# Optimization experiments

Hardware: AMD Instinct MI355X
Metric: run time of the kernel (lower is better)

## Reference

```python
import jax, jax.numpy as jnp
import numpy as np

LN_EPS = 1e-12

def setup_inputs() -> dict:
    key = jax.random.key(0)
    k1, k2 = jax.random.split(key)
    batch, seq_len, hidden, conv_size = 32, 2048, 512, 64
    input_tensor = jax.random.normal(k1, (batch, seq_len, hidden), dtype=jnp.float32)
    conv_weight = jax.random.normal(k2, (1, conv_size, hidden), dtype=jnp.float32) * 0.02
    gamma = jnp.ones((hidden,), dtype=jnp.float32)
    beta = jnp.zeros((hidden,), dtype=jnp.float32)
    return {"input_tensor": input_tensor, "conv_weight": conv_weight, "gamma": gamma, "beta": beta}

def reference(input_tensor, conv_weight, gamma, beta):
    # input_tensor: [B, S, H]; conv_weight: [1, K, H] (K << S)
    seq_len = input_tensor.shape[1]
    conv_size = conv_weight.shape[1]
    # FFT-based circular depthwise convolution along the sequence axis
    x_f = jnp.fft.rfft(input_tensor, axis=1, norm='ortho')            # [B, S//2+1, H] complex
    w_pad = jnp.pad(conv_weight, ((0, 0), (0, seq_len - conv_size), (0, 0)))  # zero-pad filter to S
    w_f = jnp.fft.rfft(w_pad, axis=1, norm='ortho')                   # [1, S//2+1, H]
    y = jnp.fft.irfft(x_f * w_f, n=seq_len, axis=1, norm='ortho')     # [B, S, H]
    # dropout is identity at inference; residual + LayerNorm(eps=1e-12)
    h = y + input_tensor
    mean = jnp.mean(h, axis=-1, keepdims=True)
    var = jnp.mean(jnp.square(h - mean), axis=-1, keepdims=True)
    return gamma * (h - mean) * jax.lax.rsqrt(var + LN_EPS) + beta
```

## Files before the change

kernel.cpp:

```cpp
#include <hip/hip_runtime.h>

#define S_LEN 2048
#define HDIM  512
#define KSZ   64
#define S_T   128
#define PH    16
#define INV_SQRT_S 0.02209708691207961f

struct Smem {
    float lh[2][PH][HDIM];
};

__device__ __forceinline__ void lds_barrier() {
    asm volatile("s_waitcnt lgkmcnt(0)\n\ts_barrier" ::: "memory");
}

template <int OFF, int BUF>
__device__ __forceinline__ void conv_phase(const float* __restrict__ xb, int sbase, int h,
                                           const float (&wr)[KSZ], float (&xw)[KSZ],
                                           float (&xp)[8], Smem* sm)
{
#pragma unroll
    for (int j = 0; j < PH; ++j) {
        const float xcur = xp[j & 7];
        xp[j & 7] = xb[((sbase + j + 8) & (S_LEN - 1)) * HDIM + h];

        float y0 = 0.f, y1 = 0.f, y2 = 0.f, y3 = 0.f;
#pragma unroll
        for (int k = 1; k <= KSZ - 7; k += 4) {
            y0 = fmaf(wr[k],     xw[(OFF + j - k)     & 63], y0);
            y1 = fmaf(wr[k + 1], xw[(OFF + j - k - 1) & 63], y1);
            y2 = fmaf(wr[k + 2], xw[(OFF + j - k - 2) & 63], y2);
            y3 = fmaf(wr[k + 3], xw[(OFF + j - k - 3) & 63], y3);
        }
        y0 = fmaf(wr[61], xw[(OFF + j - 61) & 63], y0);
        y1 = fmaf(wr[62], xw[(OFF + j - 62) & 63], y1);
        y2 = fmaf(wr[63], xw[(OFF + j - 63) & 63], y2);

        const float hval = fmaf(INV_SQRT_S, fmaf(wr[0], xcur, (y0 + y1) + (y2 + y3)), xcur);
        xw[(OFF + j) & 63] = xcur;
        sm->lh[BUF][j][h] = hval;
    }
}

template <int BUF>
__device__ __forceinline__ void ln_phase(int sbase, int lane, int wv,
                                         const float* __restrict__ gamma,
                                         const float* __restrict__ beta,
                                         float* __restrict__ ob, Smem* sm)
{
    lds_barrier();

    float gm[8], bt[8];
#pragma unroll
    for (int m = 0; m < 8; ++m) {
        gm[m] = gamma[lane + 64 * m];
        bt[m] = beta [lane + 64 * m];
    }

#pragma unroll
    for (int rr = 0; rr < 2; ++rr) {
        const int row = wv * 2 + rr;
        float v[8];
        float s = 0.f, q = 0.f;
#pragma unroll
        for (int m = 0; m < 8; ++m) {
            v[m] = sm->lh[BUF][row][lane + 64 * m];
            s += v[m];
            q = fmaf(v[m], v[m], q);
        }
#pragma unroll
        for (int d = 1; d < 64; d <<= 1) {
            s += __shfl_xor(s, d, 64);
            q += __shfl_xor(q, d, 64);
        }
        const float mean = s * (1.0f / 512.0f);
        const float rstd = rsqrtf(fmaf(q, 1.0f / 512.0f, -mean * mean) + 1e-12f);

        float* op = ob + (size_t)(sbase + row) * HDIM + lane;
#pragma unroll
        for (int m = 0; m < 8; ++m)
            op[64 * m] = fmaf(v[m] - mean, rstd * gm[m], bt[m]);
    }
}

__global__ __launch_bounds__(512, 2)
void fconv_ln(const float* __restrict__ x, const float* __restrict__ w,
              const float* __restrict__ gamma, const float* __restrict__ beta,
              float* __restrict__ out)
{
    __shared__ Smem sm;
    const int h    = threadIdx.x;
    const int lane = h & 63;
    const int wv   = h >> 6;
    const int b  = blockIdx.x >> 4;
    const int s0 = (blockIdx.x & 15) * S_T;

    const float* xb = x   + (size_t)b * S_LEN * HDIM;
    float*       ob = out + (size_t)b * S_LEN * HDIM;

    float wr[KSZ];
#pragma unroll
    for (int k = 0; k < KSZ; ++k) wr[k] = w[k * HDIM + h];

    float xw[KSZ];
#pragma unroll
    for (int d = 1; d < KSZ; ++d)
        xw[KSZ - d] = xb[((s0 - d) & (S_LEN - 1)) * HDIM + h];
    xw[0] = 0.f;

    float xp[8];
#pragma unroll
    for (int j = 0; j < 8; ++j) xp[j] = xb[(s0 + j) * HDIM + h];

    for (int grp = 0; grp < S_T / 64; ++grp) {
        const int base = s0 + grp * 64;
        conv_phase< 0, 0>(xb, base +  0, h, wr, xw, xp, &sm); ln_phase<0>(base +  0, lane, wv, gamma, beta, ob, &sm);
        conv_phase<16, 1>(xb, base + 16, h, wr, xw, xp, &sm); ln_phase<1>(base + 16, lane, wv, gamma, beta, ob, &sm);
        conv_phase<32, 0>(xb, base + 32, h, wr, xw, xp, &sm); ln_phase<0>(base + 32, lane, wv, gamma, beta, ob, &sm);
        conv_phase<48, 1>(xb, base + 48, h, wr, xw, xp, &sm); ln_phase<1>(base + 48, lane, wv, gamma, beta, ob, &sm);
    }
}

extern "C" void kernel_launch(void* const* d_in, const int* in_sizes, int n_in,
                              void* d_out, int out_size, void* d_ws, size_t ws_size,
                              hipStream_t stream) {
    const float* x  = (const float*)d_in[0];
    const float* w  = (const float*)d_in[1];
    const float* g  = (const float*)d_in[2];
    const float* b  = (const float*)d_in[3];
    float* o        = (float*)d_out;

    (void)in_sizes; (void)n_in; (void)out_size; (void)d_ws; (void)ws_size;
    fconv_ln<<<dim3(32 * (S_LEN / S_T)), dim3(HDIM), 0, stream>>>(x, w, g, b, o);
}
```

Before: 275.1 us.

## Split 64-tap depthwise conv across two half-waves with shuffle-based window handoff

Each channel is now handled by two threads in the same wavefront, each holding 32 taps and a 32-sample window, so blocks grow to 1024 threads. The sliding window passes retiring samples from the low half to the high half via cross-half shuffles, and the partial sums are combined with another shuffle. The 1/sqrt(S) scale is folded into the weights. The aim is to halve per-thread register pressure and the serial FMA chain while keeping the number of waves per CU. In exchange it adds shuffle traffic and leaves half the lanes idle during global loads and LDS stores.

```diff
diff --git a/kernel.cpp b/kernel.cpp
--- a/kernel.cpp
+++ b/kernel.cpp
@@ -2,9 +2,9 @@
 
 #define S_LEN 2048
 #define HDIM  512
-#define KSZ   64
 #define S_T   128
 #define PH    16
+#define W32   32
 #define INV_SQRT_S 0.02209708691207961f
 
 struct Smem {
@@ -16,30 +16,35 @@
 }
 
 template <int OFF, int BUF>
-__device__ __forceinline__ void conv_phase(const float* __restrict__ xb, int sbase, int h,
-                                           const float (&wr)[KSZ], float (&xw)[KSZ],
+__device__ __forceinline__ void conv_phase(const float* __restrict__ xb, int sbase,
+                                           int c, int ph,
+                                           const float (&wr)[W32], float (&xw)[W32],
                                            float (&xp)[8], Smem* sm)
 {
 #pragma unroll
     for (int j = 0; j < PH; ++j) {
         const float xcur = xp[j & 7];
-        xp[j & 7] = xb[((sbase + j + 8) & (S_LEN - 1)) * HDIM + h];
+        if (ph == 0)
+            xp[j & 7] = xb[((sbase + j + 8) & (S_LEN - 1)) * HDIM + c];
+
+        const float retire = xw[(OFF + j) & 31];
+        const float recv   = __shfl_xor(retire, 32, 64);
+        const float vins   = ph ? recv : xcur;
+        xw[(OFF + j) & 31] = vins;
 
         float y0 = 0.f, y1 = 0.f, y2 = 0.f, y3 = 0.f;
 #pragma unroll
-        for (int k = 1; k <= KSZ - 7; k += 4) {
-            y0 = fmaf(wr[k],     xw[(OFF + j - k)     & 63], y0);
-            y1 = fmaf(wr[k + 1], xw[(OFF + j - k - 1) & 63], y1);
-            y2 = fmaf(wr[k + 2], xw[(OFF + j - k - 2) & 63], y2);
-            y3 = fmaf(wr[k + 3], xw[(OFF + j - k - 3) & 63], y3);
+        for (int u = 0; u < W32; u += 4) {
+            y0 = fmaf(wr[u],     xw[(OFF + j - u)     & 31], y0);
+            y1 = fmaf(wr[u + 1], xw[(OFF + j - u - 1) & 31], y1);
+            y2 = fmaf(wr[u + 2], xw[(OFF + j - u - 2) & 31], y2);
+            y3 = fmaf(wr[u + 3], xw[(OFF + j - u - 3) & 31], y3);
         }
-        y0 = fmaf(wr[61], xw[(OFF + j - 61) & 63], y0);
-        y1 = fmaf(wr[62], xw[(OFF + j - 62) & 63], y1);
-        y2 = fmaf(wr[63], xw[(OFF + j - 63) & 63], y2);
+        float y = (y0 + y1) + (y2 + y3);
+        y += __shfl_xor(y, 32, 64);
 
-        const float hval = fmaf(INV_SQRT_S, fmaf(wr[0], xcur, (y0 + y1) + (y2 + y3)), xcur);
-        xw[(OFF + j) & 63] = xcur;
-        sm->lh[BUF][j][h] = hval;
+        if (ph == 0)
+            sm->lh[BUF][j][c] = y + xcur;
     }
 }
 
@@ -51,74 +56,71 @@
 {
     lds_barrier();
 
-    float gm[8], bt[8];
+    const int row = wv;
+    float v[8];
+    float s = 0.f, q = 0.f;
 #pragma unroll
     for (int m = 0; m < 8; ++m) {
-        gm[m] = gamma[lane + 64 * m];
-        bt[m] = beta [lane + 64 * m];
+        v[m] = sm->lh[BUF][row][lane + 64 * m];
+        s += v[m];
+        q = fmaf(v[m], v[m], q);
     }
+#pragma unroll
+    for (int d = 1; d < 64; d <<= 1) {
+        s += __shfl_xor(s, d, 64);
+        q += __shfl_xor(q, d, 64);
+    }
+    const float mean = s * (1.0f / 512.0f);
+    const float rstd = rsqrtf(fmaf(q, 1.0f / 512.0f, -mean * mean) + 1e-12f);
 
+    float* op = ob + (size_t)(sbase + row) * HDIM + lane;
 #pragma unroll
-    for (int rr = 0; rr < 2; ++rr) {
-        const int row = wv * 2 + rr;
-        float v[8];
-        float s = 0.f, q = 0.f;
-#pragma unroll
-        for (int m = 0; m < 8; ++m) {
-            v[m] = sm->lh[BUF][row][lane + 64 * m];
-            s += v[m];
-            q = fmaf(v[m], v[m], q);
-        }
-#pragma unroll
-        for (int d = 1; d < 64; d <<= 1) {
-            s += __shfl_xor(s, d, 64);
-            q += __shfl_xor(q, d, 64);
-        }
-        const float mean = s * (1.0f / 512.0f);
-        const float rstd = rsqrtf(fmaf(q, 1.0f / 512.0f, -mean * mean) + 1e-12f);
-
-        float* op = ob + (size_t)(sbase + row) * HDIM + lane;
-#pragma unroll
-        for (int m = 0; m < 8; ++m)
-            op[64 * m] = fmaf(v[m] - mean, rstd * gm[m], bt[m]);
+    for (int m = 0; m < 8; ++m) {
+        const float gm = gamma[lane + 64 * m];
+        const float bt = beta [lane + 64 * m];
+        op[64 * m] = fmaf(v[m] - mean, rstd * gm, bt);
     }
 }
 
-__global__ __launch_bounds__(512, 2)
+__global__ __launch_bounds__(1024, 1)
 void fconv_ln(const float* __restrict__ x, const float* __restrict__ w,
               const float* __restrict__ gamma, const float* __restrict__ beta,
               float* __restrict__ out)
 {
     __shared__ Smem sm;
-    const int h    = threadIdx.x;
-    const int lane = h & 63;
-    const int wv   = h >> 6;
+    const int t    = threadIdx.x;
+    const int lane = t & 63;
+    const int wv   = t >> 6;
+    const int ph   = lane >> 5;
+    const int c    = wv * 32 + (lane & 31);
     const int b  = blockIdx.x >> 4;
     const int s0 = (blockIdx.x & 15) * S_T;
 
     const float* xb = x   + (size_t)b * S_LEN * HDIM;
     float*       ob = out + (size_t)b * S_LEN * HDIM;
 
-    float wr[KSZ];
+    float wr[W32];
 #pragma unroll
-    for (int k = 0; k < KSZ; ++k) wr[k] = w[k * HDIM + h];
+    for (int u = 0; u < W32; ++u)
+        wr[u] = w[(ph * W32 + u) * HDIM + c] * INV_SQRT_S;
 
-    float xw[KSZ];
+    float xw[W32];
 #pragma unroll
-    for (int d = 1; d < KSZ; ++d)
-        xw[KSZ - d] = xb[((s0 - d) & (S_LEN - 1)) * HDIM + h];
-    xw[0] = 0.f;
+    for (int m = 0; m < W32; ++m)
+        xw[m] = xb[((s0 - ph * W32 - W32 + m) & (S_LEN - 1)) * HDIM + c];
 
     float xp[8];
 #pragma unroll
-    for (int j = 0; j < 8; ++j) xp[j] = xb[(s0 + j) * HDIM + h];
+    for (int j = 0; j < 8; ++j)
+        xp[j] = (ph == 0) ? xb[(s0 + j) * HDIM + c] : 0.f;
 
-    for (int grp = 0; grp < S_T / 64; ++grp) {
-        const int base = s0 + grp * 64;
-        conv_phase< 0, 0>(xb, base +  0, h, wr, xw, xp, &sm); ln_phase<0>(base +  0, lane, wv, gamma, beta, ob, &sm);
-        conv_phase<16, 1>(xb, base + 16, h, wr, xw, xp, &sm); ln_phase<1>(base + 16, lane, wv, gamma, beta, ob, &sm);
-        conv_phase<32, 0>(xb, base + 32, h, wr, xw, xp, &sm); ln_phase<0>(base + 32, lane, wv, gamma, beta, ob, &sm);
-        conv_phase<48, 1>(xb, base + 48, h, wr, xw, xp, &sm); ln_phase<1>(base + 48, lane, wv, gamma, beta, ob, &sm);
+#pragma unroll 1
+    for (int grp = 0; grp < 4; ++grp) {
+        const int base = s0 + grp * 32;
+        conv_phase< 0, 0>(xb, base,      c, ph, wr, xw, xp, &sm);
+        ln_phase<0>(base,      lane, wv, gamma, beta, ob, &sm);
+        conv_phase<16, 1>(xb, base + 16, c, ph, wr, xw, xp, &sm);
+        ln_phase<1>(base + 16, lane, wv, gamma, beta, ob, &sm);
     }
 }
 
@@ -132,5 +134,5 @@
     float* o        = (float*)d_out;
 
     (void)in_sizes; (void)n_in; (void)out_size; (void)d_ws; (void)ws_size;
-    fconv_ln<<<dim3(32 * (S_LEN / S_T)), dim3(HDIM), 0, stream>>>(x, w, g, b, o);
+    fconv_ln<<<dim3(32 * (S_LEN / S_T)), dim3(1024), 0, stream>>>(x, w, g, b, o);
 }
```

Measured after the change: 276.8 us. About the same (+0.6%).
